# Optimization experiments

Measured on AMD Instinct MI355X. Metric: run time of the kernel, lower is better.

Reference implementation:

```python
import jax, jax.numpy as jnp
import numpy as np

# Faithful JAX translation of fastmax_function with mask=True, p=1, normalize=0.
# In that branch the torch code sets temperature = 1 and uses a0 = a1 = 1.

def setup_inputs() -> dict:
    key = jax.random.key(0)
    kq, kk, kv = jax.random.split(key, 3)
    b, h, n, d = 2, 8, 8192, 32
    q = jax.random.normal(kq, (b, h, n, d), dtype=jnp.float32)
    k = jax.random.normal(kk, (b, h, n, d), dtype=jnp.float32)
    v = jax.random.normal(kv, (b, h, n, d), dtype=jnp.float32)
    return {"q": q, "k": k, "v": v}


def reference(q, k, v):
    # q, k, v: (b, h, n, d); causal (mask=True), p=1, a0=a1=1, temperature=1
    b, h, n, d = q.shape
    # first term: running sum of values
    first = jnp.cumsum(v, axis=2)                                  # (b,h,n,d)
    # second term: q_i . (sum_{j<=i} k_j v_j^T)
    kv = jnp.einsum('bhnd,bhne->bhnde', k, v)                      # (b,h,n,d,d)
    kv_cs = jnp.cumsum(kv, axis=2)                                 # (b,h,n,d,d)
    second = jnp.einsum('bhnd,bhnde->bhne', q, kv_cs)              # (b,h,n,d)
    # denominator: i + q_i . (sum_{j<=i} k_j)
    k_cs = jnp.cumsum(k, axis=2)                                   # (b,h,n,d)
    div1 = jnp.arange(1, n + 1, dtype=q.dtype)                     # (n,)
    div2 = jnp.einsum('bhnd,bhnd->bhn', q, k_cs)                   # (b,h,n)
    div = (div1[None, None, :] + div2)[..., None]                  # (b,h,n,1)
    return (first + second) / div
```

## Files before the change

### kernel.cpp

```cpp
#include <hip/hip_runtime.h>


#define D      32
#define C      64
#define NCHUNK 128
#define GSIZE  4
#define NGROUP 32
#define BH     16
#define NBLK   (BH * NCHUNK)
#define STATE  1088
#define STCH   1152

typedef __attribute__((ext_vector_type(8))) short bf16x8;
typedef __attribute__((ext_vector_type(4))) float f32x4;
typedef __attribute__((ext_vector_type(4))) unsigned short u16x4;

__device__ __forceinline__ unsigned short f2bf(float x) {
  union { float f; unsigned u; } c; c.f = x;
  unsigned r = (c.u + 0x7FFFu + ((c.u >> 16) & 1u)) >> 16;
  return (unsigned short)r;
}
__device__ __forceinline__ float bf2f(unsigned short u) {
  union { unsigned u; float f; } c; c.u = ((unsigned)u) << 16;
  return c.f;
}
__device__ __forceinline__ int permcol(int e) {
  return (e & 1) ? (16 + (e >> 1)) : (e >> 1);
}
__device__ __forceinline__ float4 add4(float4 a, float4 b) {
  return make_float4(a.x + b.x, a.y + b.y, a.z + b.z, a.w + b.w);
}

__global__ __launch_bounds__(256) void state_scan_kernel(
    const float* __restrict__ k, const float* __restrict__ v,
    unsigned short* __restrict__ states, float* __restrict__ totals) {
  int blk = blockIdx.x;
  int c0  = blk * GSIZE;
  const float4* kp = (const float4*)k + (size_t)c0 * 512;
  const float4* vp = (const float4*)v + (size_t)c0 * 512;

  __shared__ __align__(16) unsigned short kT[D * 72];
  __shared__ __align__(16) unsigned short vT[D * 72];
  __shared__ __align__(16) float4 psK[256];
  __shared__ __align__(16) float4 psV[256];

  int t  = threadIdx.x;
  int j0 = t >> 3;
  int cb = (t & 7) * 4;
  int lane = t & 63, w = t >> 6;
  int m16 = lane & 15, quad = lane >> 4;
  int mb = w >> 1, nb = w & 1;
  int d1b = 16 * mb + quad * 4;
  int d2  = 16 * nb + m16;
  int n   = permcol(d2);

  float pref[4] = {0.f, 0.f, 0.f, 0.f};
  float tailpref = 0.f;

  float4 kA = kp[t], kB = kp[t + 256];
  float4 vA = vp[t], vB = vp[t + 256];

  for (int ci = 0; ci < GSIZE; ++ci) {
    {
      const float* ka = &kA.x; const float* kb = &kB.x;
      const float* va = &vA.x; const float* vb = &vB.x;
#pragma unroll
      for (int cc = 0; cc < 4; ++cc) {
        kT[(cb + cc) * 72 + j0]      = f2bf(ka[cc]);
        kT[(cb + cc) * 72 + j0 + 32] = f2bf(kb[cc]);
        vT[(cb + cc) * 72 + j0]      = f2bf(va[cc]);
        vT[(cb + cc) * 72 + j0 + 32] = f2bf(vb[cc]);
      }
      psK[t] = make_float4(kA.x + kB.x, kA.y + kB.y, kA.z + kB.z, kA.w + kB.w);
      psV[t] = make_float4(vA.x + vB.x, vA.y + vB.y, vA.z + vB.z, vA.w + vB.w);
    }
    __syncthreads();

    if (ci + 1 < GSIZE) {
      const float4* kn = kp + (size_t)(ci + 1) * 512;
      const float4* vn = vp + (size_t)(ci + 1) * 512;
      kA = kn[t]; kB = kn[t + 256];
      vA = vn[t]; vB = vn[t + 256];
    }

    f32x4 acc = {0.f, 0.f, 0.f, 0.f};
#pragma unroll
    for (int kb2 = 0; kb2 < 2; ++kb2) {
      bf16x8 a = *(const bf16x8*)&kT[(16 * mb + m16) * 72 + kb2 * 32 + quad * 8];
      bf16x8 b = *(const bf16x8*)&vT[(16 * nb + m16) * 72 + kb2 * 32 + quad * 8];
      acc = __builtin_amdgcn_mfma_f32_16x16x32_bf16(a, b, acc, 0, 0, 0);
    }
    float csum = 0.f;
    if (t < 64) {
      int ee = t & 31;
      const float* ps = (t < 32) ? (const float*)psK : (const float*)psV;
#pragma unroll
      for (int m = 0; m < 32; ++m) csum += ps[ee + 32 * m];
    }

    unsigned short* stC = states + (size_t)(c0 + ci) * STCH;
    *(u16x4*)&stC[n * 32 + d1b] =
        (u16x4){f2bf(pref[0]), f2bf(pref[1]), f2bf(pref[2]), f2bf(pref[3])};
#pragma unroll
    for (int reg = 0; reg < 4; ++reg) pref[reg] += acc[reg];
    if (t < 64) {
      ((float*)(stC + 1024))[t] = tailpref;
      tailpref += csum;
    }
    __syncthreads();
  }

  float* tp = totals + (size_t)blk * STATE;
  *(float4*)&tp[n * 32 + d1b] =
      make_float4(pref[0], pref[1], pref[2], pref[3]);
  if (t < 64) tp[1024 + t] = tailpref;
}

__global__ __launch_bounds__(256, 4) void output_kernel(
    const float* __restrict__ q, const float* __restrict__ k,
    const float* __restrict__ v, const unsigned short* __restrict__ states,
    const float* __restrict__ totals, float* __restrict__ out) {
  int blk = blockIdx.x;
  int c   = blk & 127;
  int bh  = blk >> 7;
  int g   = c >> 2;
  size_t off = (size_t)blk * (C * D);
  const float4* qp4 = (const float4*)q + (size_t)blk * 512;
  const float4* kp4 = (const float4*)k + (size_t)blk * 512;
  const float4* vp4 = (const float4*)v + (size_t)blk * 512;
  const unsigned short* stc = states + (size_t)blk * STCH;
  const float* tb0 = totals + (size_t)(bh * NGROUP) * STATE;

  __shared__ __align__(16) char uA[10240];
  unsigned short* qbf = (unsigned short*)uA;
  unsigned short* kbf = (unsigned short*)(uA + 5120);
  float* q_s = (float*)uA;
  __shared__ __align__(16) unsigned short vTbf[D * 72];
  __shared__ __align__(16) unsigned short kvTbf[D * 40];
  __shared__ __align__(16) unsigned short Tbf[C * 72];
  __shared__ __align__(16) float kc_s[C * 36];
  __shared__ __align__(16) float gtot[8 * 32];
  __shared__ __align__(16) float kpre_s[D], vpre_s[D], invdiv_s[C];

  int t  = threadIdx.x;
  int j0 = t >> 3;
  int cb = (t & 7) * 4;

  float4 qA = qp4[t], qB = qp4[t + 256];
  float4 kA = kp4[t], kB = kp4[t + 256];
  float4 vA = vp4[t], vB = vp4[t + 256];
  uint2  su  = *(const uint2*)&stc[t * 4];
  float4 tv4 = make_float4(0.f, 0.f, 0.f, 0.f);
  for (int g2 = 0; g2 < g; ++g2)
    tv4 = add4(tv4, *(const float4*)&tb0[(size_t)g2 * STATE + 4 * t]);
  float4 tail = make_float4(0.f, 0.f, 0.f, 0.f);
  if (t < 16) {
    tail = *(const float4*)((const float*)(stc + 1024) + 4 * t);
    for (int g2 = 0; g2 < g; ++g2)
      tail = add4(tail, *(const float4*)&tb0[(size_t)g2 * STATE + 1024 + 4 * t]);
  }

  for (int z = t; z < (C * 72) / 8; z += 256)
    ((uint4*)Tbf)[z] = make_uint4(0, 0, 0, 0);

  *(float4*)&kc_s[j0 * 36 + cb]        = kA;
  *(float4*)&kc_s[(j0 + 32) * 36 + cb] = kB;
  *(u16x4*)&qbf[j0 * 40 + cb] =
      (u16x4){f2bf(qA.x), f2bf(qA.y), f2bf(qA.z), f2bf(qA.w)};
  *(u16x4*)&qbf[(j0 + 32) * 40 + cb] =
      (u16x4){f2bf(qB.x), f2bf(qB.y), f2bf(qB.z), f2bf(qB.w)};
  *(u16x4*)&kbf[j0 * 40 + cb] =
      (u16x4){f2bf(kA.x), f2bf(kA.y), f2bf(kA.z), f2bf(kA.w)};
  *(u16x4*)&kbf[(j0 + 32) * 40 + cb] =
      (u16x4){f2bf(kB.x), f2bf(kB.y), f2bf(kB.z), f2bf(kB.w)};
  {
    const float* va = &vA.x; const float* vb = &vB.x;
#pragma unroll
    for (int cc = 0; cc < 4; ++cc) {
      int n = permcol(cb + cc);
      vTbf[n * 72 + j0]      = f2bf(va[cc]);
      vTbf[n * 72 + j0 + 32] = f2bf(vb[cc]);
    }
  }
  {
    float s0 = bf2f((unsigned short)(su.x & 0xffff)) + tv4.x;
    float s1 = bf2f((unsigned short)(su.x >> 16))    + tv4.y;
    float s2 = bf2f((unsigned short)(su.y & 0xffff)) + tv4.z;
    float s3 = bf2f((unsigned short)(su.y >> 16))    + tv4.w;
    *(u16x4*)&kvTbf[(t >> 3) * 40 + (t & 7) * 4] =
        (u16x4){f2bf(s0), f2bf(s1), f2bf(s2), f2bf(s3)};
  }
  if (t < 8)            ((float4*)kpre_s)[t]     = tail;
  else if (t < 16)      ((float4*)vpre_s)[t - 8] = tail;
  __syncthreads();

  int lane = t & 63, w = t >> 6;
  int m16 = lane & 15, quad = lane >> 4;

  const bf16x8 aQ = *(const bf16x8*)&qbf[(16 * w + m16) * 40 + quad * 8];
  for (int jb = 0; jb <= w; ++jb) {
    bf16x8 bK = *(const bf16x8*)&kbf[(16 * jb + m16) * 40 + quad * 8];
    f32x4 cS = {0.f, 0.f, 0.f, 0.f};
    cS = __builtin_amdgcn_mfma_f32_16x16x32_bf16(aQ, bK, cS, 0, 0, 0);
    int jcol = 16 * jb + m16;
#pragma unroll
    for (int reg = 0; reg < 4; ++reg) {
      int i = 16 * w + quad * 4 + reg;
      float tv = (jcol <= i) ? (1.f + cS[reg]) : 0.f;
      Tbf[i * 72 + jcol] = f2bf(tv);
    }
  }
  int rg = t >> 5;
  int e  = t & 31;
  float vals[8];
  {
    float run = 0.f;
#pragma unroll
    for (int r = 0; r < 8; ++r) {
      vals[r] = kc_s[(rg * 8 + r) * 36 + e];
      run += vals[r];
    }
    gtot[rg * 32 + e] = run;
  }
  __syncthreads();

  {
    float offv = kpre_s[e];
    for (int g2 = 0; g2 < rg; ++g2) offv += gtot[g2 * 32 + e];
    float cacc = offv;
#pragma unroll
    for (int r = 0; r < 8; ++r) {
      cacc += vals[r];
      kc_s[(rg * 8 + r) * 36 + e] = cacc;
    }
  }
  *(float4*)&q_s[j0 * 36 + cb]        = qA;
  *(float4*)&q_s[(j0 + 32) * 36 + cb] = qB;
  __syncthreads();

  if (t < 64) {
    int i = t;
    float dp = 0.f;
#pragma unroll
    for (int d4 = 0; d4 < 8; ++d4) {
      float4 qv = *(const float4*)&q_s[i * 36 + 4 * d4];
      float4 kc = *(const float4*)&kc_s[i * 36 + 4 * d4];
      dp += qv.x * kc.x + qv.y * kc.y + qv.z * kc.z + qv.w * kc.w;
    }
    invdiv_s[i] = 1.f / ((float)(c * C + i + 1) + dp);
  }
  f32x4 o0 = {0.f, 0.f, 0.f, 0.f}, o1 = {0.f, 0.f, 0.f, 0.f};
  {
    bf16x8 b0 = *(const bf16x8*)&kvTbf[(m16)      * 40 + quad * 8];
    bf16x8 b1 = *(const bf16x8*)&kvTbf[(16 + m16) * 40 + quad * 8];
    o0 = __builtin_amdgcn_mfma_f32_16x16x32_bf16(aQ, b0, o0, 0, 0, 0);
    o1 = __builtin_amdgcn_mfma_f32_16x16x32_bf16(aQ, b1, o1, 0, 0, 0);
  }
  int kbcnt = (w >= 2) ? 2 : 1;
  for (int kb2 = 0; kb2 < kbcnt; ++kb2) {
    bf16x8 aT = *(const bf16x8*)&Tbf[(16 * w + m16) * 72 + kb2 * 32 + quad * 8];
    bf16x8 b0 = *(const bf16x8*)&vTbf[(m16)      * 72 + kb2 * 32 + quad * 8];
    bf16x8 b1 = *(const bf16x8*)&vTbf[(16 + m16) * 72 + kb2 * 32 + quad * 8];
    o0 = __builtin_amdgcn_mfma_f32_16x16x32_bf16(aT, b0, o0, 0, 0, 0);
    o1 = __builtin_amdgcn_mfma_f32_16x16x32_bf16(aT, b1, o1, 0, 0, 0);
  }
  __syncthreads();

  int e0 = 2 * m16;
#pragma unroll
  for (int reg = 0; reg < 4; ++reg) {
    int i = 16 * w + quad * 4 + reg;
    float id = invdiv_s[i];
    float2 o;
    o.x = (vpre_s[e0]     + o0[reg]) * id;
    o.y = (vpre_s[e0 + 1] + o1[reg]) * id;
    *(float2*)&out[off + (size_t)i * D + e0] = o;
  }
}

extern "C" void kernel_launch(void* const* d_in, const int* in_sizes, int n_in,
                              void* d_out, int out_size, void* d_ws, size_t ws_size,
                              hipStream_t stream) {
  const float* q = (const float*)d_in[0];
  const float* k = (const float*)d_in[1];
  const float* v = (const float*)d_in[2];
  float* out = (float*)d_out;
  unsigned short* states = (unsigned short*)d_ws;
  float* totals = (float*)(states + (size_t)NBLK * STCH);

  state_scan_kernel<<<BH * NGROUP, 256, 0, stream>>>(k, v, states, totals);
  output_kernel<<<NBLK, 256, 0, stream>>>(q, k, v, states, totals, out);
}
```

Before: 119.7 us.

## Split state scan into per-chunk KV kernel plus separate column-wise prefix scan

Replaces the grouped state scan and the per-block summation of preceding group totals with three stages. A per-chunk kernel computes each chunk's k^T v and column sums into fp32 totals, a dedicated kernel turns these into exclusive prefixes along the chunk axis, and the output kernel reads one precomputed prefix per chunk. This removes the O(g) redundant reads of group totals in the output kernel and the bf16 intra-group state. The cost is an extra launch and a serial 128-step scan per state element, and the prefixes are now held in fp32 rather than bf16.

```diff
diff --git a/kernel.cpp b/kernel.cpp
--- a/kernel.cpp
+++ b/kernel.cpp
@@ -4,12 +4,9 @@
 #define D      32
 #define C      64
 #define NCHUNK 128
-#define GSIZE  4
-#define NGROUP 32
 #define BH     16
 #define NBLK   (BH * NCHUNK)
 #define STATE  1088
-#define STCH   1152
 
 typedef __attribute__((ext_vector_type(8))) short bf16x8;
 typedef __attribute__((ext_vector_type(4))) float f32x4;
@@ -20,24 +17,16 @@
   unsigned r = (c.u + 0x7FFFu + ((c.u >> 16) & 1u)) >> 16;
   return (unsigned short)r;
 }
-__device__ __forceinline__ float bf2f(unsigned short u) {
-  union { unsigned u; float f; } c; c.u = ((unsigned)u) << 16;
-  return c.f;
-}
 __device__ __forceinline__ int permcol(int e) {
   return (e & 1) ? (16 + (e >> 1)) : (e >> 1);
 }
-__device__ __forceinline__ float4 add4(float4 a, float4 b) {
-  return make_float4(a.x + b.x, a.y + b.y, a.z + b.z, a.w + b.w);
-}
-
-__global__ __launch_bounds__(256) void state_scan_kernel(
+
+__global__ __launch_bounds__(256) void chunk_kv_kernel(
     const float* __restrict__ k, const float* __restrict__ v,
-    unsigned short* __restrict__ states, float* __restrict__ totals) {
+    float* __restrict__ totals) {
   int blk = blockIdx.x;
-  int c0  = blk * GSIZE;
-  const float4* kp = (const float4*)k + (size_t)c0 * 512;
-  const float4* vp = (const float4*)v + (size_t)c0 * 512;
+  const float4* kp = (const float4*)k + (size_t)blk * 512;
+  const float4* vp = (const float4*)v + (size_t)blk * 512;
 
   __shared__ __align__(16) unsigned short kT[D * 72];
   __shared__ __align__(16) unsigned short vT[D * 72];
@@ -54,82 +43,69 @@
   int d2  = 16 * nb + m16;
   int n   = permcol(d2);
 
-  float pref[4] = {0.f, 0.f, 0.f, 0.f};
-  float tailpref = 0.f;
-
   float4 kA = kp[t], kB = kp[t + 256];
   float4 vA = vp[t], vB = vp[t + 256];
 
-  for (int ci = 0; ci < GSIZE; ++ci) {
-    {
-      const float* ka = &kA.x; const float* kb = &kB.x;
-      const float* va = &vA.x; const float* vb = &vB.x;
-#pragma unroll
-      for (int cc = 0; cc < 4; ++cc) {
-        kT[(cb + cc) * 72 + j0]      = f2bf(ka[cc]);
-        kT[(cb + cc) * 72 + j0 + 32] = f2bf(kb[cc]);
-        vT[(cb + cc) * 72 + j0]      = f2bf(va[cc]);
-        vT[(cb + cc) * 72 + j0 + 32] = f2bf(vb[cc]);
-      }
-      psK[t] = make_float4(kA.x + kB.x, kA.y + kB.y, kA.z + kB.z, kA.w + kB.w);
-      psV[t] = make_float4(vA.x + vB.x, vA.y + vB.y, vA.z + vB.z, vA.w + vB.w);
-    }
-    __syncthreads();
-
-    if (ci + 1 < GSIZE) {
-      const float4* kn = kp + (size_t)(ci + 1) * 512;
-      const float4* vn = vp + (size_t)(ci + 1) * 512;
-      kA = kn[t]; kB = kn[t + 256];
-      vA = vn[t]; vB = vn[t + 256];
-    }
-
-    f32x4 acc = {0.f, 0.f, 0.f, 0.f};
-#pragma unroll
-    for (int kb2 = 0; kb2 < 2; ++kb2) {
-      bf16x8 a = *(const bf16x8*)&kT[(16 * mb + m16) * 72 + kb2 * 32 + quad * 8];
-      bf16x8 b = *(const bf16x8*)&vT[(16 * nb + m16) * 72 + kb2 * 32 + quad * 8];
-      acc = __builtin_amdgcn_mfma_f32_16x16x32_bf16(a, b, acc, 0, 0, 0);
-    }
+  {
+    const float* ka = &kA.x; const float* kb = &kB.x;
+    const float* va = &vA.x; const float* vb = &vB.x;
+#pragma unroll
+    for (int cc = 0; cc < 4; ++cc) {
+      kT[(cb + cc) * 72 + j0]      = f2bf(ka[cc]);
+      kT[(cb + cc) * 72 + j0 + 32] = f2bf(kb[cc]);
+      vT[(cb + cc) * 72 + j0]      = f2bf(va[cc]);
+      vT[(cb + cc) * 72 + j0 + 32] = f2bf(vb[cc]);
+    }
+    psK[t] = make_float4(kA.x + kB.x, kA.y + kB.y, kA.z + kB.z, kA.w + kB.w);
+    psV[t] = make_float4(vA.x + vB.x, vA.y + vB.y, vA.z + vB.z, vA.w + vB.w);
+  }
+  __syncthreads();
+
+  f32x4 acc = {0.f, 0.f, 0.f, 0.f};
+#pragma unroll
+  for (int kb2 = 0; kb2 < 2; ++kb2) {
+    bf16x8 a = *(const bf16x8*)&kT[(16 * mb + m16) * 72 + kb2 * 32 + quad * 8];
+    bf16x8 b = *(const bf16x8*)&vT[(16 * nb + m16) * 72 + kb2 * 32 + quad * 8];
+    acc = __builtin_amdgcn_mfma_f32_16x16x32_bf16(a, b, acc, 0, 0, 0);
+  }
+
+  float* tp = totals + (size_t)blk * STATE;
+  *(float4*)&tp[n * 32 + d1b] = make_float4(acc[0], acc[1], acc[2], acc[3]);
+  if (t < 64) {
+    int ee = t & 31;
+    const float* ps = (t < 32) ? (const float*)psK : (const float*)psV;
     float csum = 0.f;
-    if (t < 64) {
-      int ee = t & 31;
-      const float* ps = (t < 32) ? (const float*)psK : (const float*)psV;
-#pragma unroll
-      for (int m = 0; m < 32; ++m) csum += ps[ee + 32 * m];
-    }
-
-    unsigned short* stC = states + (size_t)(c0 + ci) * STCH;
-    *(u16x4*)&stC[n * 32 + d1b] =
-        (u16x4){f2bf(pref[0]), f2bf(pref[1]), f2bf(pref[2]), f2bf(pref[3])};
-#pragma unroll
-    for (int reg = 0; reg < 4; ++reg) pref[reg] += acc[reg];
-    if (t < 64) {
-      ((float*)(stC + 1024))[t] = tailpref;
-      tailpref += csum;
-    }
-    __syncthreads();
-  }
-
-  float* tp = totals + (size_t)blk * STATE;
-  *(float4*)&tp[n * 32 + d1b] =
-      make_float4(pref[0], pref[1], pref[2], pref[3]);
-  if (t < 64) tp[1024 + t] = tailpref;
+#pragma unroll
+    for (int m = 0; m < 32; ++m) csum += ps[ee + 32 * m];
+    tp[1024 + t] = csum;
+  }
+}
+
+__global__ __launch_bounds__(256) void totals_scan_kernel(float* __restrict__ totals) {
+  int gidx = blockIdx.x * 256 + threadIdx.x;
+  int bh = gidx / STATE;
+  int e  = gidx % STATE;
+  float* base = totals + (size_t)(bh * NCHUNK) * STATE + e;
+  float a = 0.f;
+#pragma unroll 8
+  for (int cc = 0; cc < NCHUNK; ++cc) {
+    float s = base[(size_t)cc * STATE];
+    base[(size_t)cc * STATE] = a;
+    a += s;
+  }
 }
 
 __global__ __launch_bounds__(256, 4) void output_kernel(
     const float* __restrict__ q, const float* __restrict__ k,
-    const float* __restrict__ v, const unsigned short* __restrict__ states,
-    const float* __restrict__ totals, float* __restrict__ out) {
+    const float* __restrict__ v, const float* __restrict__ totals,
+    float* __restrict__ out) {
   int blk = blockIdx.x;
   int c   = blk & 127;
-  int bh  = blk >> 7;
-  int g   = c >> 2;
   size_t off = (size_t)blk * (C * D);
   const float4* qp4 = (const float4*)q + (size_t)blk * 512;
   const float4* kp4 = (const float4*)k + (size_t)blk * 512;
   const float4* vp4 = (const float4*)v + (size_t)blk * 512;
-  const unsigned short* stc = states + (size_t)blk * STCH;
-  const float* tb0 = totals + (size_t)(bh * NGROUP) * STATE;
+  const float* tbc = totals + (size_t)blk * STATE;
 
   __shared__ __align__(16) char uA[10240];
   unsigned short* qbf = (unsigned short*)uA;
@@ -149,16 +125,9 @@
   float4 qA = qp4[t], qB = qp4[t + 256];
   float4 kA = kp4[t], kB = kp4[t + 256];
   float4 vA = vp4[t], vB = vp4[t + 256];
-  uint2  su  = *(const uint2*)&stc[t * 4];
-  float4 tv4 = make_float4(0.f, 0.f, 0.f, 0.f);
-  for (int g2 = 0; g2 < g; ++g2)
-    tv4 = add4(tv4, *(const float4*)&tb0[(size_t)g2 * STATE + 4 * t]);
+  float4 tv4 = *(const float4*)&tbc[4 * t];
   float4 tail = make_float4(0.f, 0.f, 0.f, 0.f);
-  if (t < 16) {
-    tail = *(const float4*)((const float*)(stc + 1024) + 4 * t);
-    for (int g2 = 0; g2 < g; ++g2)
-      tail = add4(tail, *(const float4*)&tb0[(size_t)g2 * STATE + 1024 + 4 * t]);
-  }
+  if (t < 16) tail = *(const float4*)&tbc[1024 + 4 * t];
 
   for (int z = t; z < (C * 72) / 8; z += 256)
     ((uint4*)Tbf)[z] = make_uint4(0, 0, 0, 0);
@@ -182,14 +151,8 @@
       vTbf[n * 72 + j0 + 32] = f2bf(vb[cc]);
     }
   }
-  {
-    float s0 = bf2f((unsigned short)(su.x & 0xffff)) + tv4.x;
-    float s1 = bf2f((unsigned short)(su.x >> 16))    + tv4.y;
-    float s2 = bf2f((unsigned short)(su.y & 0xffff)) + tv4.z;
-    float s3 = bf2f((unsigned short)(su.y >> 16))    + tv4.w;
-    *(u16x4*)&kvTbf[(t >> 3) * 40 + (t & 7) * 4] =
-        (u16x4){f2bf(s0), f2bf(s1), f2bf(s2), f2bf(s3)};
-  }
+  *(u16x4*)&kvTbf[(t >> 3) * 40 + (t & 7) * 4] =
+      (u16x4){f2bf(tv4.x), f2bf(tv4.y), f2bf(tv4.z), f2bf(tv4.w)};
   if (t < 8)            ((float4*)kpre_s)[t]     = tail;
   else if (t < 16)      ((float4*)vpre_s)[t - 8] = tail;
   __syncthreads();
@@ -285,9 +248,9 @@
   const float* k = (const float*)d_in[1];
   const float* v = (const float*)d_in[2];
   float* out = (float*)d_out;
-  unsigned short* states = (unsigned short*)d_ws;
-  float* totals = (float*)(states + (size_t)NBLK * STCH);
-
-  state_scan_kernel<<<BH * NGROUP, 256, 0, stream>>>(k, v, states, totals);
-  output_kernel<<<NBLK, 256, 0, stream>>>(q, k, v, states, totals, out);
-}
+  float* totals = (float*)d_ws;
+
+  chunk_kv_kernel<<<NBLK, 256, 0, stream>>>(k, v, totals);
+  totals_scan_kernel<<<(BH * STATE) / 256, 256, 0, stream>>>(totals);
+  output_kernel<<<NBLK, 256, 0, stream>>>(q, k, v, totals, out);
+}
```

Result: faster. 109.6 us (-8.4%).
